# Performance work log

Measured on AMD Instinct MI355X. Metric: run time of the kernel, lower is better.

Reference implementation:

```python
import jax, jax.numpy as jnp
import numpy as np

E, HE, HD, V, B, S, T = 512, 1024, 1024, 32000, 64, 48, 48
PAD = 0


def lstm_cell(x, h, c, Wih, Whh, b):
    # torch gate order: i, f, g, o
    g = x @ Wih.T + h @ Whh.T + b
    i, f, gg, o = jnp.split(g, 4, axis=-1)
    c2 = jax.nn.sigmoid(f) * c + jax.nn.sigmoid(i) * jnp.tanh(gg)
    h2 = jax.nn.sigmoid(o) * jnp.tanh(c2)
    return h2, c2


def run_lstm(X, mask, Wih, Whh, b):
    # X: [S,B,E], mask: [S,B] bool; emulates packed-sequence semantics:
    # carry frozen and output zeroed at padded steps.
    hsz = Whh.shape[1]
    h0 = jnp.zeros((X.shape[1], hsz), X.dtype)

    def step(carry, xm):
        h, c = carry
        x, m = xm
        h2, c2 = lstm_cell(x, h, c, Wih, Whh, b)
        m = m[:, None]
        h = jnp.where(m, h2, h)
        c = jnp.where(m, c2, c)
        return (h, c), h * m

    (hT, cT), outs = jax.lax.scan(step, (h0, h0), (X, mask))
    return outs, hT, cT


def setup_inputs() -> dict:
    key = jax.random.key(0)
    ks = jax.random.split(key, 24)

    def rn(k, shape, scale=0.05):
        return jax.random.normal(k, shape, jnp.float32) * scale

    inp = {}
    inp['source_padded'] = jax.random.randint(ks[0], (S, B), 1, V).astype(jnp.int32)
    inp['target_padded'] = jax.random.randint(ks[1], (T, B), 1, V).astype(jnp.int32)
    lens = jnp.sort(jax.random.randint(ks[2], (B,), S // 2, S + 1))[::-1]
    inp['source_lengths'] = lens.at[0].set(S).astype(jnp.int32)
    # embeddings (padding row zeroed, matching nn.Embedding padding_idx)
    inp['src_emb'] = rn(ks[3], (V, E)).at[PAD].set(0.0)
    inp['tgt_emb'] = rn(ks[4], (V, E)).at[PAD].set(0.0)
    # bidirectional encoder LSTM (b = b_ih + b_hh combined)
    inp['enc_Wih_f'] = rn(ks[5], (4 * HE, E))
    inp['enc_Whh_f'] = rn(ks[6], (4 * HE, HE))
    inp['enc_b_f'] = rn(ks[7], (4 * HE,))
    inp['enc_Wih_b'] = rn(ks[8], (4 * HE, E))
    inp['enc_Whh_b'] = rn(ks[9], (4 * HE, HE))
    inp['enc_b_b'] = rn(ks[10], (4 * HE,))
    # decoder LSTMCell
    inp['dec_Wih'] = rn(ks[11], (4 * HD, E + HD))
    inp['dec_Whh'] = rn(ks[12], (4 * HD, HD))
    inp['dec_b'] = rn(ks[13], (4 * HD,))
    # projections (all bias=False in the original)
    inp['W_h'] = rn(ks[14], (HD, 2 * HE))
    inp['W_c'] = rn(ks[15], (HD, 2 * HE))
    inp['W_att'] = rn(ks[16], (HD, 2 * HE))
    inp['W_comb'] = rn(ks[17], (HE, 2 * HE + HD))
    inp['W_vocab'] = rn(ks[18], (V, HD))
    return inp


def reference(source_padded, target_padded, source_lengths, src_emb, tgt_emb,
              enc_Wih_f, enc_Whh_f, enc_b_f, enc_Wih_b, enc_Whh_b, enc_b_b,
              dec_Wih, dec_Whh, dec_b, W_h, W_c, W_att, W_comb, W_vocab):
    # ---- encode ----
    X = src_emb[source_padded]                       # [S,B,E]
    tpos = jnp.arange(S)[:, None]
    valid = tpos < source_lengths[None, :]           # [S,B]
    fwd_out, h_f, c_f = run_lstm(X, valid, enc_Wih_f, enc_Whh_f, enc_b_f)
    # reverse each sequence within its true length (packed-seq backward dir)
    rev_idx = jnp.where(valid, source_lengths[None, :] - 1 - tpos, tpos)
    Xrev = jnp.take_along_axis(X, rev_idx[:, :, None], axis=0)
    bwd_rev, h_b, c_b = run_lstm(Xrev, valid, enc_Wih_b, enc_Whh_b, enc_b_b)
    bwd_out = jnp.take_along_axis(bwd_rev, rev_idx[:, :, None], axis=0)
    enc_hiddens = jnp.concatenate([fwd_out, bwd_out], -1).transpose(1, 0, 2)  # [B,S,2HE]
    dec_h0 = jnp.concatenate([h_f, h_b], -1) @ W_h.T  # [B,HD]
    dec_c0 = jnp.concatenate([c_f, c_b], -1) @ W_c.T
    # ---- decode ----
    enc_proj = enc_hiddens @ W_att.T                 # [B,S,HD]
    pad_mask = ~valid.T                              # [B,S], True at padding
    Y = tgt_emb[target_padded[:-1]]                  # [T-1,B,E]

    def dstep(o_prev, y):
        ybar = jnp.concatenate([y, o_prev], -1)
        # NOTE: faithful to source bug - step() is always called with
        # dec_init_state, so the LSTMCell state resets every timestep.
        h_t, c_t = lstm_cell(ybar, dec_h0, dec_c0, dec_Wih, dec_Whh, dec_b)
        e = jnp.einsum('bsh,bh->bs', enc_proj, h_t)  # multiplicative attention
        e = jnp.where(pad_mask, -jnp.inf, e)
        alpha = jax.nn.softmax(e, -1)
        a = jnp.einsum('bs,bsd->bd', alpha, enc_hiddens)   # [B,2HE]
        O = jnp.tanh(jnp.concatenate([a, h_t], -1) @ W_comb.T)  # dropout=identity (eval)
        return O, O

    o0 = jnp.zeros((B, HD), X.dtype)
    _, combined = jax.lax.scan(dstep, o0, Y)          # [T-1,B,HE]
    # ---- loss-style scores ----
    P = jax.nn.log_softmax(combined @ W_vocab.T, -1)  # [T-1,B,V]
    gold = jnp.take_along_axis(P, target_padded[1:][:, :, None], axis=-1)[..., 0]
    tmask = (target_padded[1:] != PAD).astype(P.dtype)
    return (gold * tmask).sum(0)                      # [B]
```

## Files before the change

kernel.cpp:

```cpp
#include <hip/hip_runtime.h>
#include <math.h>


#define S_    48
#define B_    64
#define E_    512
#define H_    1024
#define H4_   4096
#define V_    32000
#define T1_   47
#define NROW_ 3008
#define NROWP 3072
#define NTV_  500
#define NBE   128
#define NBD   128

typedef __bf16 bf16x8 __attribute__((ext_vector_type(8)));
typedef float  f32x4  __attribute__((ext_vector_type(4)));
typedef unsigned short ushort_t;
typedef unsigned long long ull_t;

__device__ __forceinline__ float sigm(float x){ return 1.f/(1.f+expf(-x)); }
__device__ __forceinline__ unsigned short f2bs(float f){
  unsigned u=__float_as_uint(f); u+=0x7fffu+((u>>16)&1u); return (unsigned short)(u>>16);
}
__device__ __forceinline__ float b2f(ushort_t u){ return __uint_as_float(((unsigned)u)<<16); }
__device__ __forceinline__ void gload16(const ushort_t* g, ushort_t* l){
  __builtin_amdgcn_global_load_lds((const __attribute__((address_space(1))) void*)g,
                                   (__attribute__((address_space(3))) void*)l,16,0,0);
}

__device__ __forceinline__ void ast32(void* p, unsigned v){
  __hip_atomic_store((unsigned*)p,v,__ATOMIC_RELAXED,__HIP_MEMORY_SCOPE_AGENT);
}
__device__ __forceinline__ void ast64(void* p, ull_t v){
  __hip_atomic_store((ull_t*)p,v,__ATOMIC_RELAXED,__HIP_MEMORY_SCOPE_AGENT);
}

__device__ __forceinline__ void arrive(unsigned* flags, int idx, unsigned ep){
  if(threadIdx.x==0) ast32(&flags[idx*16], ep);
}
__device__ __forceinline__ void wait_flags(unsigned* flags, int n, unsigned ep){
  for(int i=threadIdx.x;i<n;i+=256){
    while(__hip_atomic_load(&flags[i*16],__ATOMIC_RELAXED,__HIP_MEMORY_SCOPE_AGENT)<ep)
      __builtin_amdgcn_s_sleep(1);
  }
  __syncthreads();
}

__device__ __forceinline__ void stage128(const ushort_t* src, int ld, int k0,
                                         ushort_t* lds, int w, int lane){
  const int rA=lane>>3, gA=lane&7;
#pragma unroll
  for(int i=0;i<4;i++){
    int rb=w*32+i*8;
    int row=rb+rA;
    gload16(src+(size_t)row*ld+k0+(((gA)^(row&7))*8), &lds[rb*64]);
  }
}
__device__ __forceinline__ void stage256(const ushort_t* src, int ld, int k0,
                                         ushort_t* lds, int w, int lane){
#pragma unroll
  for(int p=0;p<2;p++){
    int s0=p*1024+w*64;
    int s=s0+lane;
    int row=s>>3, g=s&7;
    gload16(src+(size_t)row*ld+k0+((g^(row&7))*8), &lds[(size_t)s0*8]);
  }
}

#define ACC_DECL \
  f32x4 c00={0,0,0,0},c01={0,0,0,0},c02={0,0,0,0},c03={0,0,0,0}, \
        c10={0,0,0,0},c11={0,0,0,0},c12={0,0,0,0},c13={0,0,0,0}, \
        c20={0,0,0,0},c21={0,0,0,0},c22={0,0,0,0},c23={0,0,0,0}, \
        c30={0,0,0,0},c31={0,0,0,0},c32={0,0,0,0},c33={0,0,0,0};

#define MFMA_ __builtin_amdgcn_mfma_f32_16x16x32_bf16
#define MMA_K64(AsB,BsB) do{ \
  _Pragma("unroll") \
  for(int ks_=0;ks_<2;ks_++){ \
    const int sw_=((ks_*4+l4)^l7)*8; \
    bf16x8 a0_=*(const bf16x8*)&(AsB)[(wm*64+ 0+l15)*64+sw_]; \
    bf16x8 a1_=*(const bf16x8*)&(AsB)[(wm*64+16+l15)*64+sw_]; \
    bf16x8 a2_=*(const bf16x8*)&(AsB)[(wm*64+32+l15)*64+sw_]; \
    bf16x8 a3_=*(const bf16x8*)&(AsB)[(wm*64+48+l15)*64+sw_]; \
    bf16x8 b0_=*(const bf16x8*)&(BsB)[(wn*64+ 0+l15)*64+sw_]; \
    bf16x8 b1_=*(const bf16x8*)&(BsB)[(wn*64+16+l15)*64+sw_]; \
    bf16x8 b2_=*(const bf16x8*)&(BsB)[(wn*64+32+l15)*64+sw_]; \
    bf16x8 b3_=*(const bf16x8*)&(BsB)[(wn*64+48+l15)*64+sw_]; \
    c00=MFMA_(a0_,b0_,c00,0,0,0); c01=MFMA_(a0_,b1_,c01,0,0,0); \
    c02=MFMA_(a0_,b2_,c02,0,0,0); c03=MFMA_(a0_,b3_,c03,0,0,0); \
    c10=MFMA_(a1_,b0_,c10,0,0,0); c11=MFMA_(a1_,b1_,c11,0,0,0); \
    c12=MFMA_(a1_,b2_,c12,0,0,0); c13=MFMA_(a1_,b3_,c13,0,0,0); \
    c20=MFMA_(a2_,b0_,c20,0,0,0); c21=MFMA_(a2_,b1_,c21,0,0,0); \
    c22=MFMA_(a2_,b2_,c22,0,0,0); c23=MFMA_(a2_,b3_,c23,0,0,0); \
    c30=MFMA_(a3_,b0_,c30,0,0,0); c31=MFMA_(a3_,b1_,c31,0,0,0); \
    c32=MFMA_(a3_,b2_,c32,0,0,0); c33=MFMA_(a3_,b3_,c33,0,0,0); \
  } \
}while(0)

__global__ __launch_bounds__(256)
void proj3(const ushort_t* __restrict__ Xb, const ushort_t* __restrict__ WfB, const float* __restrict__ bf,
           const ushort_t* __restrict__ XrB, const ushort_t* __restrict__ WbB, const float* __restrict__ bb,
           const ushort_t* __restrict__ Yb, const ushort_t* __restrict__ WyB,
           ushort_t* __restrict__ XpF, ushort_t* __restrict__ XpB, ushort_t* __restrict__ Yp)
{
  __shared__ __align__(16) ushort_t As[128*64];
  __shared__ __align__(16) ushort_t Bs[128*64];
  const ushort_t* A; const ushort_t* B; const float* bias; ushort_t* C;
  if(blockIdx.z==0){A=Xb;B=WfB;bias=bf;C=XpF;}
  else if(blockIdx.z==1){A=XrB;B=WbB;bias=bb;C=XpB;}
  else {A=Yb;B=WyB;bias=nullptr;C=Yp;}
  const int tid=threadIdx.x, w=tid>>6, lane=tid&63;
  const int wm=w>>1, wn=w&1;
  const int l15=lane&15, l4=lane>>4, l7=lane&7;
  const int m0=blockIdx.x*128, n0=blockIdx.y*128;
  ACC_DECL
  for(int k0=0;k0<E_;k0+=64){
    stage128(A+(size_t)m0*E_, E_, k0, As, w, lane);
    stage128(B+(size_t)n0*E_, E_, k0, Bs, w, lane);
    __syncthreads();
    MMA_K64(As,Bs);
    __syncthreads();
  }
  const int cr=l4*4, cc=l15;
#define PSTORE(CM,mi,ni) { int col=n0+wn*64+(ni)*16+cc; float bv=bias?bias[col]:0.f; \
  _Pragma("unroll") for(int j=0;j<4;j++){ int row=m0+wm*64+(mi)*16+cr+j; \
    C[(size_t)row*H4_+col]=f2bs(CM[j]+bv); } }
  PSTORE(c00,0,0) PSTORE(c01,0,1) PSTORE(c02,0,2) PSTORE(c03,0,3)
  PSTORE(c10,1,0) PSTORE(c11,1,1) PSTORE(c12,1,2) PSTORE(c13,1,3)
  PSTORE(c20,2,0) PSTORE(c21,2,1) PSTORE(c22,2,2) PSTORE(c23,2,3)
  PSTORE(c30,3,0) PSTORE(c31,3,1) PSTORE(c32,3,2) PSTORE(c33,3,3)
#undef PSTORE
}

__global__ __launch_bounds__(256)
void bproj(const ushort_t* __restrict__ A, int lda,
           const ushort_t* __restrict__ B, int ldb, int K,
           ushort_t* __restrict__ Cb)
{
  __shared__ __align__(16) ushort_t As[128*64];
  __shared__ __align__(16) ushort_t Bs[128*64];
  const int tid=threadIdx.x, w=tid>>6, lane=tid&63;
  const int wm=w>>1, wn=w&1;
  const int l15=lane&15, l4=lane>>4, l7=lane&7;
  const int m0=blockIdx.x*128, n0=blockIdx.y*128;
  ACC_DECL
  for(int k0=0;k0<K;k0+=64){
    stage128(A+(size_t)m0*lda, lda, k0, As, w, lane);
    stage128(B+(size_t)n0*ldb, ldb, k0, Bs, w, lane);
    __syncthreads();
    MMA_K64(As,Bs);
    __syncthreads();
  }
  const int cr=l4*4, cc=l15;
#define BSTORE(CM,mi,ni) { int col=n0+wn*64+(ni)*16+cc; \
  _Pragma("unroll") for(int j=0;j<4;j++){ int row=m0+wm*64+(mi)*16+cr+j; \
    Cb[(size_t)row*H_+col]=f2bs(CM[j]); } }
  BSTORE(c00,0,0) BSTORE(c01,0,1) BSTORE(c02,0,2) BSTORE(c03,0,3)
  BSTORE(c10,1,0) BSTORE(c11,1,1) BSTORE(c12,1,2) BSTORE(c13,1,3)
  BSTORE(c20,2,0) BSTORE(c21,2,1) BSTORE(c22,2,2) BSTORE(c23,2,3)
  BSTORE(c30,3,0) BSTORE(c31,3,1) BSTORE(c32,3,2) BSTORE(c33,3,3)
#undef BSTORE
}

__global__ __launch_bounds__(1024)
void mfma_vocab(const ushort_t* __restrict__ A, const ushort_t* __restrict__ B,
                const int* __restrict__ tgt,
                float* __restrict__ pmax, float* __restrict__ psum, float* __restrict__ gold)
{
  __shared__ __align__(16) ushort_t As[256*64];
  __shared__ __align__(16) ushort_t Bs[256*64];
  const int tid=threadIdx.x, w=tid>>6, lane=tid&63;
  const int wm=w>>2, wn=w&3;
  const int l15=lane&15, l4=lane>>4, l7=lane&7;
  const int m0=blockIdx.x*256, n0=blockIdx.y*256;
  ACC_DECL
  for(int k0=0;k0<H_;k0+=64){
    stage256(A+(size_t)m0*H_, H_, k0, As, w, lane);
    stage256(B+(size_t)n0*H_, H_, k0, Bs, w, lane);
    __syncthreads();
    MMA_K64(As,Bs);
    __syncthreads();
  }
  const int tile=blockIdx.y*4+wn;
  const int cc=l15;
#define VEPI(mi,R0,R1,R2,R3) { \
  _Pragma("unroll") for(int j=0;j<4;j++){ \
    int row=m0+wm*64+(mi)*16+l4*4+j; \
    float m=fmaxf(fmaxf(R0[j],R1[j]),fmaxf(R2[j],R3[j])); \
    for(int o=1;o<16;o<<=1) m=fmaxf(m,__shfl_xor(m,o,64)); \
    float s=expf(R0[j]-m)+expf(R1[j]-m)+expf(R2[j]-m)+expf(R3[j]-m); \
    for(int o=1;o<16;o<<=1) s+=__shfl_xor(s,o,64); \
    if(row<NROW_){ \
      if(cc==0){ pmax[(size_t)tile*NROWP+row]=m; psum[(size_t)tile*NROWP+row]=s; } \
      int g=tgt[((row>>6)+1)*B_+(row&63)]; \
      int lj=g-(n0+wn*64); \
      if(lj>=0&&lj<64&&(lj&15)==cc){ int q=lj>>4; \
        gold[row]= (q==0)?R0[j]:(q==1)?R1[j]:(q==2)?R2[j]:R3[j]; } \
    } } }
  VEPI(0,c00,c01,c02,c03)
  VEPI(1,c10,c11,c12,c13)
  VEPI(2,c20,c21,c22,c23)
  VEPI(3,c30,c31,c32,c33)
#undef VEPI
}

__global__ __launch_bounds__(256)
void enc_persist(const ushort_t* __restrict__ WhhB2,
                 const ushort_t* __restrict__ XpF, const ushort_t* __restrict__ XpB,
                 const int* __restrict__ lens,
                 ushort_t* __restrict__ hroll,
                 float* __restrict__ cst,
                 ushort_t* __restrict__ outF, ushort_t* __restrict__ outBR,
                 unsigned* __restrict__ flagsE)
{
  __shared__ __align__(16) ushort_t Bp[64*1024];
  const int tid=threadIdx.x, w=tid>>6, lane=tid&63;
  const int blk=blockIdx.x, dir=blk>>6, j0=(blk&63)*16;
  const int l15=lane&15, l4=lane>>4;
  const ushort_t* Wd=WhhB2+(size_t)dir*H4_*H_;
  const ushort_t* xp = dir? XpB : XpF;
  float* cD = cst + (size_t)dir*65536;
  ushort_t* outD = dir? outBR : outF;
  unsigned* fD = flagsE + dir*64*16;

  for(int p=0;p<32;p++){
    int s=p*256+w*64+lane;
    int row=s>>7, g=s&127;
    int grow=((row>>4)<<10)+j0+(row&15);
    gload16(Wd+(size_t)grow*H_+((g^(row&7))*8), &Bp[(p*256+w*64)*8]);
  }
  __syncthreads();

  float hkeep[4]={0.f,0.f,0.f,0.f};

  for(int t=0;t<S_;t++){
    const ushort_t* hbR = hroll + ((size_t)t*2+dir)*65536;
    ushort_t*       hbW = hroll + ((size_t)(t+1)*2+dir)*65536;
    bf16x8 a[32];
    {
      const ushort_t* ap=hbR+(size_t)(w*16+l15)*H_+l4*8;
#pragma unroll
      for(int kk=0;kk<32;kk++) a[kk]=*(const bf16x8*)(ap+kk*32);
    }
    f32x4 acc[4];
#pragma unroll
    for(int n=0;n<4;n++) acc[n]=(f32x4){0.f,0.f,0.f,0.f};
#pragma unroll
    for(int kk=0;kk<32;kk++){
#pragma unroll
      for(int n=0;n<4;n++){
        int rb=n*16+l15;
        bf16x8 b=*(const bf16x8*)&Bp[rb*H_+(((kk*4+l4)^(rb&7))*8)];
        acc[n]=__builtin_amdgcn_mfma_f32_16x16x32_bf16(a[kk],b,acc[n],0,0,0);
      }
    }
    const int col=j0+l15;
#pragma unroll
    for(int j=0;j<4;j++){
      int row=w*16+l4*4+j;
      const ushort_t* xr=xp+(size_t)(t*64+row)*H4_;
      float g0=acc[0][j]+b2f(xr[col]);
      float g1=acc[1][j]+b2f(xr[1024+col]);
      float g2=acc[2][j]+b2f(xr[2048+col]);
      float g3=acc[3][j]+b2f(xr[3072+col]);
      size_t ix=(size_t)row*H_+col;
      float c_old=cD[ix];
      float cn=sigm(g1)*c_old+sigm(g0)*tanhf(g2);
      float hv=sigm(g3)*tanhf(cn);
      bool m=t<lens[row];
      cD[ix]= m? cn : c_old;
      hkeep[j]= m? hv : hkeep[j];
      outD[(size_t)(t*64+row)*H_+col]= m? f2bs(hv) : (ushort_t)0;
      ushort_t h16=f2bs(hkeep[j]);
      ushort_t other=(ushort_t)__shfl_xor((int)h16,1,64);
      if((lane&1)==0)
        ast32((void*)(hbW+ix), (unsigned)h16 | ((unsigned)other<<16));
    }
    __syncthreads();
    arrive(fD, blk&63, (unsigned)(t+1));
    wait_flags(fD, 64, (unsigned)(t+1));
  }
}

__global__ __launch_bounds__(256)
void dec_persist(const ushort_t* __restrict__ WoB,
                 const ushort_t* __restrict__ Yp,
                 const float* __restrict__ whhC,
                 const float* __restrict__ dc0,
                 const ushort_t* __restrict__ encPb,
                 const ushort_t* __restrict__ Gb,
                 const ushort_t* __restrict__ WcombB,
                 const int* __restrict__ lens,
                 ushort_t* __restrict__ opRoll,
                 ushort_t* __restrict__ hRoll,
                 float* __restrict__ accRoll,
                 ushort_t* __restrict__ combB,
                 unsigned* __restrict__ fA,
                 unsigned* __restrict__ fB,
                 unsigned* __restrict__ fM)
{
  __shared__ __align__(16) ushort_t Bp[32*1024];
  __shared__ __align__(16) ushort_t WcHp[16*1024];
  __shared__ float gbuf[64*32];
  __shared__ float whhCs[64*32];
  __shared__ float dc0s[64*8];
  __shared__ float es[S_], al[S_];
  const int tid=threadIdx.x, w=tid>>6, lane=tid&63;
  const int blk=blockIdx.x;
  const int l15=lane&15, l4=lane>>4;
  const int j0=blk*8;
  const int b=blk;
  const int j0c=(blk-64)*16;

  for(int p=0;p<16;p++){
    int s=p*256+w*64+lane;
    int row=s>>7, g=s&127;
    int grow=((row>>3)<<10)+j0+(row&7);
    gload16(WoB+(size_t)grow*H_+((g^(row&7))*8), &Bp[(p*256+w*64)*8]);
  }
  if(blk>=64){
    for(int p=0;p<8;p++){
      int s=p*256+w*64+lane;
      int row=s>>7, g=s&127;
      gload16(WcombB+(size_t)(j0c+row)*3072+2048+((g^(row&7))*8), &WcHp[(p*256+w*64)*8]);
    }
  }
  for(int p=0;p<8;p++){
    int s=p*256+tid;
    int row=s>>5, gc=s&31, gate=gc>>3, c=gc&7;
    whhCs[s]=whhC[(size_t)row*H4_+gate*1024+j0+c];
  }
  if(tid<512){ int row=tid>>3, c=tid&7; dc0s[tid]=dc0[(size_t)row*H_+j0+c]; }
  __syncthreads();

  for(int t=0;t<T1_;t++){
    const unsigned ept=(unsigned)(t+1);
    const ushort_t* opT = opRoll + (size_t)t*65536;
    ushort_t*       opW = opRoll + (size_t)(t+1)*65536;
    ushort_t*       hT  = hRoll  + (size_t)t*65536;
    float*          accT= accRoll+ (size_t)t*65536;
    {
      bf16x8 a[32];
      {
        const ushort_t* ap=opT+(size_t)(w*16+l15)*H_+l4*8;
#pragma unroll
        for(int kk=0;kk<32;kk++) a[kk]=*(const bf16x8*)(ap+kk*32);
      }
      f32x4 acc0=(f32x4){0.f,0.f,0.f,0.f}, acc1=(f32x4){0.f,0.f,0.f,0.f};
#pragma unroll
      for(int kk=0;kk<32;kk++){
        int rb0=l15, rb1=16+l15;
        bf16x8 b0=*(const bf16x8*)&Bp[rb0*1024+(((kk*4+l4)^(rb0&7))*8)];
        bf16x8 b1=*(const bf16x8*)&Bp[rb1*1024+(((kk*4+l4)^(rb1&7))*8)];
        acc0=__builtin_amdgcn_mfma_f32_16x16x32_bf16(a[kk],b0,acc0,0,0,0);
        acc1=__builtin_amdgcn_mfma_f32_16x16x32_bf16(a[kk],b1,acc1,0,0,0);
      }
#pragma unroll
      for(int j=0;j<4;j++){
        gbuf[(w*16+l4*4+j)*32 + l15   ]=acc0[j];
        gbuf[(w*16+l4*4+j)*32 + 16+l15]=acc1[j];
      }
      __syncthreads();
      {
        int o=tid*2, row=o>>3, c=o&7;
        const ushort_t* ypr=Yp+(size_t)(t*64+row)*H4_;
        float hv2[2];
#pragma unroll
        for(int q=0;q<2;q++){
          int cc=c+q;
          float g0=gbuf[row*32+cc]   +b2f(ypr[j0+cc])     +whhCs[row*32+cc];
          float g1=gbuf[row*32+8+cc] +b2f(ypr[1024+j0+cc])+whhCs[row*32+8+cc];
          float g2=gbuf[row*32+16+cc]+b2f(ypr[2048+j0+cc])+whhCs[row*32+16+cc];
          float g3=gbuf[row*32+24+cc]+b2f(ypr[3072+j0+cc])+whhCs[row*32+24+cc];
          float cn=sigm(g1)*dc0s[row*8+cc]+sigm(g0)*tanhf(g2);
          hv2[q]=sigm(g3)*tanhf(cn);
        }
        unsigned pk=(unsigned)f2bs(hv2[0]) | ((unsigned)f2bs(hv2[1])<<16);
        ast32((void*)(hT+(size_t)row*H_+j0+c), pk);
      }
    }
    __syncthreads();
    arrive(fA, blk, ept);
    wait_flags(fA, 128, ept);

    if(blk<64){
      float hreg[16];
      {
        const ushort_t* hp=hT+(size_t)b*H_+lane*16;
        bf16x8 h0=*(const bf16x8*)hp, h1=*(const bf16x8*)(hp+8);
#pragma unroll
        for(int i=0;i<8;i++){ hreg[i]=b2f(((const ushort_t*)&h0)[i]);
                              hreg[8+i]=b2f(((const ushort_t*)&h1)[i]); }
      }
      for(int s=w;s<S_;s+=4){
        const ushort_t* epr=encPb+((size_t)b*S_+s)*H_+lane*16;
        bf16x8 e0=*(const bf16x8*)epr, e1=*(const bf16x8*)(epr+8);
        float sum=0.f;
#pragma unroll
        for(int i=0;i<8;i++) sum+=b2f(((const ushort_t*)&e0)[i])*hreg[i]
                                +b2f(((const ushort_t*)&e1)[i])*hreg[8+i];
        for(int o=32;o>0;o>>=1) sum+=__shfl_xor(sum,o,64);
        if(lane==0) es[s]=sum;
      }
      __syncthreads();
      if(tid<64){
        int L=lens[b];
        float e=(tid<S_&&tid<L)? es[tid] : -INFINITY;
        float m=e;
        for(int o=32;o>0;o>>=1) m=fmaxf(m,__shfl_xor(m,o,64));
        float p=(tid<S_)? expf(e-m):0.f;
        float sm=p;
        for(int o=32;o>0;o>>=1) sm+=__shfl_xor(sm,o,64);
        if(tid<S_) al[tid]=p/sm;
      }
      __syncthreads();
      float r0=0.f,r1=0.f,r2=0.f,r3=0.f;
      const int c4=tid*4;
      for(int s=0;s<S_;s++){
        float aa=al[s];
        ushort4 g4=*(const ushort4*)(Gb+((size_t)b*S_+s)*H_+c4);
        r0+=aa*b2f(g4.x); r1+=aa*b2f(g4.y); r2+=aa*b2f(g4.z); r3+=aa*b2f(g4.w);
      }
      wait_flags(fM, 64, ept);
      {
        float4 ap4=*(const float4*)(accT+(size_t)b*H_+c4);
        float o0=tanhf(r0+ap4.x);
        float o1=tanhf(r1+ap4.y);
        float o2=tanhf(r2+ap4.z);
        float o3=tanhf(r3+ap4.w);
        ushort_t b0=f2bs(o0),b1=f2bs(o1),b2_=f2bs(o2),b3=f2bs(o3);
        ull_t pk=(ull_t)b0 | ((ull_t)b1<<16) | ((ull_t)b2_<<32) | ((ull_t)b3<<48);
        ast64((void*)(opW+(size_t)b*H_+c4), pk);
        ushort4 cb; cb.x=b0; cb.y=b1; cb.z=b2_; cb.w=b3;
        *(ushort4*)(combB+((size_t)t*64+b)*H_+c4)=cb;
      }
      __syncthreads();
      arrive(fB, blk, ept);
      wait_flags(fB, 64, ept);
    } else {
      bf16x8 a[32];
      {
        const ushort_t* ap=hT+(size_t)(w*16+l15)*H_+l4*8;
#pragma unroll
        for(int kk=0;kk<32;kk++) a[kk]=*(const bf16x8*)(ap+kk*32);
      }
      f32x4 accP=(f32x4){0.f,0.f,0.f,0.f};
#pragma unroll
      for(int kk=0;kk<32;kk++){
        bf16x8 bb=*(const bf16x8*)&WcHp[l15*1024+(((kk*4+l4)^(l15&7))*8)];
        accP=__builtin_amdgcn_mfma_f32_16x16x32_bf16(a[kk],bb,accP,0,0,0);
      }
#pragma unroll
      for(int j=0;j<4;j++){
        int row=w*16+l4*4+j, col=j0c+l15;
        float v=accP[j];
        float other=__shfl_xor(v,1,64);
        if((lane&1)==0){
          union{ float f[2]; ull_t q; } u; u.f[0]=v; u.f[1]=other;
          ast64((void*)(accT+(size_t)row*H_+col), u.q);
        }
      }
      __syncthreads();
      arrive(fM, blk-64, ept);
      wait_flags(fB, 64, ept);
    }
  }
}

__global__ void embed_all(const int* __restrict__ src, const int* __restrict__ tgt,
                          const int* __restrict__ lens,
                          const float* __restrict__ se, const float* __restrict__ te,
                          ushort_t* __restrict__ X, ushort_t* __restrict__ Xr,
                          ushort_t* __restrict__ Y)
{
  int bi=blockIdx.x, tid=threadIdx.x;
  const float* srcrow; ushort_t* dst;
  if(bi<3072){
    int s=bi>>6, b=bi&63;
    srcrow=se+(size_t)src[s*64+b]*E_; dst=X+(size_t)bi*E_;
  } else if(bi<6144){
    int r=bi-3072, t=r>>6, b=r&63;
    int L=lens[b]; int ts=(t<L)? L-1-t : t;
    srcrow=se+(size_t)src[ts*64+b]*E_; dst=Xr+(size_t)r*E_;
  } else {
    int r=bi-6144, t=r>>6, b=r&63;
    srcrow=te+(size_t)tgt[t*64+b]*E_; dst=Y+(size_t)r*E_;
  }
  float4 v=((const float4*)srcrow)[tid];
  ushort4 o; o.x=f2bs(v.x); o.y=f2bs(v.y); o.z=f2bs(v.z); o.w=f2bs(v.w);
  ((ushort4*)dst)[tid]=o;
}

__global__ void prep_w(const float* __restrict__ Whhf,const float* __restrict__ Whhb,
                       const float* __restrict__ Wihf,const float* __restrict__ Wihb,
                       const float* __restrict__ Watt,const float* __restrict__ dWih,
                       const float* __restrict__ Wcomb,
                       ushort_t* __restrict__ WhhfB,ushort_t* __restrict__ WhhbB,
                       ushort_t* __restrict__ WihfB,ushort_t* __restrict__ WihbB,
                       ushort_t* __restrict__ WattB,ushort_t* __restrict__ dWihYb,
                       ushort_t* __restrict__ dWihOb,ushort_t* __restrict__ WcombB)
{
  const int NQ=6029312;
  for(int q=blockIdx.x*256+threadIdx.x; q<NQ; q+=gridDim.x*256){
    const float* src; ushort_t* dst; size_t si,di; int r;
    if(q<1048576){ si=(size_t)q*4; src=Whhf; dst=WhhfB; di=si; }
    else if(q<2097152){ r=q-1048576; si=(size_t)r*4; src=Whhb; dst=WhhbB; di=si; }
    else if(q<2621440){ r=q-2097152; si=(size_t)r*4; src=Wihf; dst=WihfB; di=si; }
    else if(q<3145728){ r=q-2621440; si=(size_t)r*4; src=Wihb; dst=WihbB; di=si; }
    else if(q<3670016){ r=q-3145728; si=(size_t)r*4; src=Watt; dst=WattB; di=si; }
    else if(q<4194304){ r=q-3670016; int row=r>>7, c4=(r&127)*4;
                        si=(size_t)row*1536+c4; src=dWih; dst=dWihYb; di=(size_t)row*512+c4; }
    else if(q<5242880){ r=q-4194304; int row=r>>8, c4=(r&255)*4;
                        si=(size_t)row*1536+512+c4; src=dWih; dst=dWihOb; di=(size_t)row*1024+c4; }
    else { r=q-5242880; si=(size_t)r*4; src=Wcomb; dst=WcombB; di=si; }
    float4 v=*(const float4*)(src+si);
    ushort4 o; o.x=f2bs(v.x);o.y=f2bs(v.y);o.z=f2bs(v.z);o.w=f2bs(v.w);
    *(ushort4*)(dst+di)=o;
  }
}

__global__ void f2b_voc(const float* __restrict__ in, ushort_t* __restrict__ out){
  for(size_t q=blockIdx.x*256+threadIdx.x; q<8192000; q+=(size_t)gridDim.x*256){
    float4 v=*(const float4*)(in+q*4);
    ushort4 o; o.x=f2bs(v.x);o.y=f2bs(v.y);o.z=f2bs(v.z);o.w=f2bs(v.w);
    *(ushort4*)(out+q*4)=o;
  }
}

__global__ void gather_concat(const ushort_t* __restrict__ outF, const ushort_t* __restrict__ outBR,
                              const int* __restrict__ lens,
                              const ushort_t* __restrict__ hb, const float* __restrict__ cst,
                              ushort_t* __restrict__ encHb,
                              float* __restrict__ hcat, float* __restrict__ ccat)
{
  int bi=blockIdx.x, tid=threadIdx.x;
  if(bi<3072){
    int b=bi/48, s=bi%48;
    int L=lens[b]; int sr=(s<L)? L-1-s : s;
    ((ushort4*)(encHb+(size_t)bi*2048))[tid]      =((const ushort4*)(outF +(size_t)(s*64+b)*H_))[tid];
    ((ushort4*)(encHb+(size_t)bi*2048+1024))[tid] =((const ushort4*)(outBR+(size_t)(sr*64+b)*H_))[tid];
  } else {
    int b=bi-3072;
    for(int i=tid;i<H_;i+=256){
      hcat[(size_t)b*2048+i]      = b2f(hb[(size_t)b*H_+i]);
      hcat[(size_t)b*2048+1024+i] = b2f(hb[65536+(size_t)b*H_+i]);
      ccat[(size_t)b*2048+i]      = cst[(size_t)b*H_+i];
      ccat[(size_t)b*2048+1024+i] = cst[65536+(size_t)b*H_+i];
    }
  }
}

template<int BM,int BN,int TM,int TN>
__global__ __launch_bounds__(256)
void gemm_nt(int M, int K,
             const float* __restrict__ A, int lda,
             const float* __restrict__ B, int ldb,
             float* __restrict__ C, int ldc,
             const float* __restrict__ bias)
{
  constexpr int BK=16;
  __shared__ float As[BK][BM+4];
  __shared__ float Bs[BK][BN+4];
  const int tid=threadIdx.x;
  constexpr int TX=BN/TN;
  const int tx=tid%TX, ty=tid/TX;
  const int m0=blockIdx.x*BM, n0=blockIdx.y*BN;
  float acc[TM][TN];
#pragma unroll
  for(int i=0;i<TM;i++)
#pragma unroll
    for(int j=0;j<TN;j++) acc[i][j]=0.f;
  for(int k0=0;k0<K;k0+=BK){
    for(int i=tid;i<BM*4;i+=256){
      int r=i>>2, c=(i&3)*4;
      float4 v=make_float4(0.f,0.f,0.f,0.f);
      if(m0+r<M) v=*(const float4*)(A+(size_t)(m0+r)*lda+k0+c);
      As[c+0][r]=v.x; As[c+1][r]=v.y; As[c+2][r]=v.z; As[c+3][r]=v.w;
    }
    for(int i=tid;i<BN*4;i+=256){
      int r=i>>2, c=(i&3)*4;
      float4 v=*(const float4*)(B+(size_t)(n0+r)*ldb+k0+c);
      Bs[c+0][r]=v.x; Bs[c+1][r]=v.y; Bs[c+2][r]=v.z; Bs[c+3][r]=v.w;
    }
    __syncthreads();
#pragma unroll
    for(int k=0;k<BK;k++){
      float a[TM], bb[TN];
#pragma unroll
      for(int i=0;i<TM;i++) a[i]=As[k][ty*TM+i];
#pragma unroll
      for(int j=0;j<TN;j++) bb[j]=Bs[k][tx*TN+j];
#pragma unroll
      for(int i=0;i<TM;i++)
#pragma unroll
        for(int j=0;j<TN;j++) acc[i][j]+=a[i]*bb[j];
    }
    __syncthreads();
  }
#pragma unroll
  for(int i=0;i<TM;i++){
    int r=m0+ty*TM+i;
    if(r>=M) continue;
#pragma unroll
    for(int j=0;j<TN;j++){
      int c=n0+tx*TN+j;
      float v=acc[i][j];
      if(bias) v+=bias[c];
      C[(size_t)r*ldc+c]=v;
    }
  }
}

__global__ __launch_bounds__(256)
void lse_final(const float* __restrict__ pmax, const float* __restrict__ psum,
               const float* __restrict__ gold, float* __restrict__ gl)
{
  int r=blockIdx.x*256+threadIdx.x;
  if(r>=NROW_) return;
  float M=-INFINITY, S=0.f;
  for(int i=0;i<NTV_;i++){
    float m2=pmax[(size_t)i*NROWP+r];
    float s2=psum[(size_t)i*NROWP+r];
    float Mn=fmaxf(M,m2);
    S = S*expf(M-Mn) + s2*expf(m2-Mn);
    M=Mn;
  }
  gl[r]=gold[r]-(M+logf(S));
}

__global__ void final_sum(const float* __restrict__ gl, const int* __restrict__ tgt,
                          float* __restrict__ out)
{
  int b=threadIdx.x;
  float acc=0.f;
  for(int t=0;t<T1_;t++){
    int tk=tgt[(t+1)*B_+b];
    if(tk!=0) acc+=gl[t*B_+b];
  }
  out[b]=acc;
}

extern "C" void kernel_launch(void* const* d_in, const int* in_sizes, int n_in,
                              void* d_out, int out_size, void* d_ws, size_t ws_size,
                              hipStream_t stream)
{
  (void)in_sizes; (void)n_in; (void)out_size; (void)ws_size;
  const int*   src    =(const int*)  d_in[0];
  const int*   tgt    =(const int*)  d_in[1];
  const int*   lens   =(const int*)  d_in[2];
  const float* src_emb=(const float*)d_in[3];
  const float* tgt_emb=(const float*)d_in[4];
  const float* Wih_f  =(const float*)d_in[5];
  const float* Whh_f  =(const float*)d_in[6];
  const float* b_f    =(const float*)d_in[7];
  const float* Wih_b  =(const float*)d_in[8];
  const float* Whh_b  =(const float*)d_in[9];
  const float* b_b    =(const float*)d_in[10];
  const float* dWih   =(const float*)d_in[11];
  const float* dWhh   =(const float*)d_in[12];
  const float* db     =(const float*)d_in[13];
  const float* W_h    =(const float*)d_in[14];
  const float* W_c    =(const float*)d_in[15];
  const float* W_att  =(const float*)d_in[16];
  const float* W_comb =(const float*)d_in[17];
  const float* W_voc  =(const float*)d_in[18];
  float* out=(float*)d_out;
  float* W  =(float*)d_ws;

  size_t off=0;
  auto AL=[&](size_t n){ size_t o=off; off+=n; return o; };
  const size_t oXpF  =AL((size_t)3072*H4_);
  const size_t oXpB  =AL((size_t)3072*H4_);
  const size_t oYp   =AL((size_t)3072*H4_);
  const size_t oCst  =AL((size_t)2*64*H_);
  const size_t oHcat =AL((size_t)64*2048);
  const size_t oCcat =AL((size_t)64*2048);
  const size_t oDh0  =AL((size_t)64*H_);
  const size_t oDc0  =AL((size_t)64*H_);
  const size_t oWhhC =AL((size_t)64*H4_);
  const size_t oBar  =AL((size_t)8192);
  const size_t oXb    =AL((size_t)3072*E_/2);
  const size_t oXrb   =AL((size_t)3072*E_/2);
  const size_t oYb    =AL((size_t)3072*E_/2);
  const size_t oWhhfB =AL((size_t)H4_*H_/2);
  const size_t oWhhbB =AL((size_t)H4_*H_/2);
  const size_t oWihfB =AL((size_t)H4_*E_/2);
  const size_t oWihbB =AL((size_t)H4_*E_/2);
  const size_t oWattB =AL((size_t)H_*2048/2);
  const size_t odWihYb=AL((size_t)H4_*E_/2);
  const size_t odWihOb=AL((size_t)H4_*H_/2);
  const size_t oWcombB=AL((size_t)H_*3072/2);
  const size_t oOutF  =AL((size_t)S_*64*H_/2);
  const size_t oOutBR =AL((size_t)S_*64*H_/2);
  const size_t oEncHb =AL((size_t)3072*2048/2);
  const size_t oEncPb =AL((size_t)3072*H_/2);

  ushort_t* Xb    =(ushort_t*)(W+oXb);
  ushort_t* Xrb   =(ushort_t*)(W+oXrb);
  ushort_t* Yb    =(ushort_t*)(W+oYb);
  ushort_t* WhhfB =(ushort_t*)(W+oWhhfB);
  ushort_t* WihfB =(ushort_t*)(W+oWihfB);
  ushort_t* WihbB =(ushort_t*)(W+oWihbB);
  ushort_t* WattB =(ushort_t*)(W+oWattB);
  ushort_t* dWihYb=(ushort_t*)(W+odWihYb);
  ushort_t* dWihOb=(ushort_t*)(W+odWihOb);
  ushort_t* WcombB=(ushort_t*)(W+oWcombB);
  ushort_t* OutF  =(ushort_t*)(W+oOutF);
  ushort_t* OutBR =(ushort_t*)(W+oOutBR);
  ushort_t* EncHb =(ushort_t*)(W+oEncHb);
  ushort_t* EncPb =(ushort_t*)(W+oEncPb);
  ushort_t* XpFb  =(ushort_t*)(W+oXpF);
  ushort_t* XpBb  =(ushort_t*)(W+oXpB);
  ushort_t* YpB   =(ushort_t*)(W+oYp);
  float*    AccRoll = W+oYp+6300000;
  ushort_t* WvocB =(ushort_t*)(W+oXpF);
  float* pmax = W+oXpF+16450000;
  float* psum = pmax + (size_t)NTV_*NROWP;
  ushort_t* Gbuf  =(ushort_t*)(W+oXpF+19550000);
  ushort_t* OpRoll=(ushort_t*)(W+oXpF+21150000);
  ushort_t* HRoll =(ushort_t*)(W+oXpF+22750000);
  float* gold = W+oXpF+24400000;
  float* gl   = gold + NROWP;
  ushort_t* HrollE=EncHb;
  ushort_t* HbFin =HrollE+(size_t)S_*2*65536;
  ushort_t* CombB =(ushort_t*)(W+oOutF);
  unsigned* flagsE=(unsigned*)(W+oBar);
  unsigned* fA = flagsE + 2*64*16;
  unsigned* fB = fA + 128*16;
  unsigned* fM = fB + 64*16;

  hipMemsetAsync(W+oBar, 0, 8192*sizeof(float), stream);
  hipMemsetAsync(W+oCst, 0, (size_t)2*64*H_*sizeof(float), stream);
  hipMemsetAsync(HrollE, 0, (size_t)2*65536*sizeof(ushort_t), stream);

  embed_all<<<dim3(3072+3072+NROW_),128,0,stream>>>(src,tgt,lens,src_emb,tgt_emb,Xb,Xrb,Yb);
  prep_w<<<dim3(2048),256,0,stream>>>(Whh_f,Whh_b,Wih_f,Wih_b,W_att,dWih,W_comb,
                                      WhhfB,(ushort_t*)(W+oWhhbB),WihfB,WihbB,WattB,
                                      dWihYb,dWihOb,WcombB);
  proj3<<<dim3(24,32,3),256,0,stream>>>(Xb,WihfB,b_f, Xrb,WihbB,b_b, Yb,dWihYb,
                                        XpFb,XpBb,YpB);

  enc_persist<<<dim3(NBE),256,0,stream>>>(WhhfB, XpFb, XpBb, lens,
                                          HrollE, W+oCst, OutF, OutBR, flagsE);

  hipMemsetAsync(OpRoll, 0, (size_t)65536*sizeof(ushort_t), stream);

  gather_concat<<<dim3(3136),256,0,stream>>>(OutF,OutBR,lens,HbFin,W+oCst,
                                             EncHb,W+oHcat,W+oCcat);
  f2b_voc<<<dim3(2048),256,0,stream>>>(W_voc, WvocB);
  bproj<<<dim3(24,8),256,0,stream>>>(EncHb,2048, WattB,2048, 2048, EncPb);
  bproj<<<dim3(24,8),256,0,stream>>>(EncHb,2048, WcombB,3072, 2048, Gbuf);
  gemm_nt<64,64,4,4><<<dim3(1,16),256,0,stream>>>(64,2048, W+oHcat,2048, W_h,2048, W+oDh0,H_, nullptr);
  gemm_nt<64,64,4,4><<<dim3(1,16),256,0,stream>>>(64,2048, W+oCcat,2048, W_c,2048, W+oDc0,H_, nullptr);
  gemm_nt<64,64,4,4><<<dim3(1,64),256,0,stream>>>(64,H_, W+oDh0,H_, dWhh,H_, W+oWhhC,H4_, db);

  dec_persist<<<dim3(NBD),256,0,stream>>>(dWihOb, YpB, W+oWhhC, W+oDc0,
                                          EncPb, Gbuf, WcombB, lens,
                                          OpRoll, HRoll, AccRoll, CombB, fA, fB, fM);

  mfma_vocab<<<dim3(12,125),1024,0,stream>>>(CombB, WvocB, tgt, pmax, psum, gold);
  lse_final<<<dim3((NROW_+255)/256),256,0,stream>>>(pmax, psum, gold, gl);
  final_sum<<<dim3(1),64,0,stream>>>(gl, tgt, out);
}
```

Baseline: 2.214 ms.

## Fuse vocab projection into persistent decoder kernel to overlap with recurrence

Removes the separate mfma_vocab launch and adds 125 extra blocks to dec_persist. Each of these blocks owns a 256-column stripe of the vocab weight and, once a decoder step's flag is published, computes that step's 64-row logits tile with its partial max, sum and gold values. The aim is to hide the large vocab GEMM behind the sequential decoder recurrence instead of running it afterwards. The combined-output store becomes an atomic 64-bit store so the consumer blocks see it. The risks are that the vocab blocks re-stream the whole vocab weight every step (47 times in total) rather than reusing it across rows, they compete with the latency-critical decoder blocks for bandwidth, and the persistent grid now depends on all 253 blocks being co-resident.

```diff
diff --git a/kernel.cpp b/kernel.cpp
--- a/kernel.cpp
+++ b/kernel.cpp
@@ -14,6 +14,7 @@
 #define NTV_  500
 #define NBE   128
 #define NBD   128
+#define NVB   125
 
 typedef __bf16 bf16x8 __attribute__((ext_vector_type(8)));
 typedef float  f32x4  __attribute__((ext_vector_type(4)));
@@ -56,16 +57,6 @@
     int rb=w*32+i*8;
     int row=rb+rA;
     gload16(src+(size_t)row*ld+k0+(((gA)^(row&7))*8), &lds[rb*64]);
-  }
-}
-__device__ __forceinline__ void stage256(const ushort_t* src, int ld, int k0,
-                                         ushort_t* lds, int w, int lane){
-#pragma unroll
-  for(int p=0;p<2;p++){
-    int s0=p*1024+w*64;
-    int s=s0+lane;
-    int row=s>>3, g=s&7;
-    gload16(src+(size_t)row*ld+k0+((g^(row&7))*8), &lds[(size_t)s0*8]);
   }
 }
 
@@ -164,48 +155,6 @@
 #undef BSTORE
 }
 
-__global__ __launch_bounds__(1024)
-void mfma_vocab(const ushort_t* __restrict__ A, const ushort_t* __restrict__ B,
-                const int* __restrict__ tgt,
-                float* __restrict__ pmax, float* __restrict__ psum, float* __restrict__ gold)
-{
-  __shared__ __align__(16) ushort_t As[256*64];
-  __shared__ __align__(16) ushort_t Bs[256*64];
-  const int tid=threadIdx.x, w=tid>>6, lane=tid&63;
-  const int wm=w>>2, wn=w&3;
-  const int l15=lane&15, l4=lane>>4, l7=lane&7;
-  const int m0=blockIdx.x*256, n0=blockIdx.y*256;
-  ACC_DECL
-  for(int k0=0;k0<H_;k0+=64){
-    stage256(A+(size_t)m0*H_, H_, k0, As, w, lane);
-    stage256(B+(size_t)n0*H_, H_, k0, Bs, w, lane);
-    __syncthreads();
-    MMA_K64(As,Bs);
-    __syncthreads();
-  }
-  const int tile=blockIdx.y*4+wn;
-  const int cc=l15;
-#define VEPI(mi,R0,R1,R2,R3) { \
-  _Pragma("unroll") for(int j=0;j<4;j++){ \
-    int row=m0+wm*64+(mi)*16+l4*4+j; \
-    float m=fmaxf(fmaxf(R0[j],R1[j]),fmaxf(R2[j],R3[j])); \
-    for(int o=1;o<16;o<<=1) m=fmaxf(m,__shfl_xor(m,o,64)); \
-    float s=expf(R0[j]-m)+expf(R1[j]-m)+expf(R2[j]-m)+expf(R3[j]-m); \
-    for(int o=1;o<16;o<<=1) s+=__shfl_xor(s,o,64); \
-    if(row<NROW_){ \
-      if(cc==0){ pmax[(size_t)tile*NROWP+row]=m; psum[(size_t)tile*NROWP+row]=s; } \
-      int g=tgt[((row>>6)+1)*B_+(row&63)]; \
-      int lj=g-(n0+wn*64); \
-      if(lj>=0&&lj<64&&(lj&15)==cc){ int q=lj>>4; \
-        gold[row]= (q==0)?R0[j]:(q==1)?R1[j]:(q==2)?R2[j]:R3[j]; } \
-    } } }
-  VEPI(0,c00,c01,c02,c03)
-  VEPI(1,c10,c11,c12,c13)
-  VEPI(2,c20,c21,c22,c23)
-  VEPI(3,c30,c31,c32,c33)
-#undef VEPI
-}
-
 __global__ __launch_bounds__(256)
 void enc_persist(const ushort_t* __restrict__ WhhB2,
                  const ushort_t* __restrict__ XpF, const ushort_t* __restrict__ XpB,
@@ -297,6 +246,10 @@
                  ushort_t* __restrict__ hRoll,
                  float* __restrict__ accRoll,
                  ushort_t* __restrict__ combB,
+                 const ushort_t* __restrict__ WvocB,
+                 const int* __restrict__ tgt,
+                 float* __restrict__ pmax, float* __restrict__ psum,
+                 float* __restrict__ gold,
                  unsigned* __restrict__ fA,
                  unsigned* __restrict__ fB,
                  unsigned* __restrict__ fM)
@@ -309,7 +262,59 @@
   __shared__ float es[S_], al[S_];
   const int tid=threadIdx.x, w=tid>>6, lane=tid&63;
   const int blk=blockIdx.x;
-  const int l15=lane&15, l4=lane>>4;
+  const int l15=lane&15, l4=lane>>4, l7=lane&7;
+
+  if(blk>=NBD){
+    const int stripe=blk-NBD;
+    ushort_t* As=(ushort_t*)Bp;
+    ushort_t* Bs=((ushort_t*)Bp)+64*64;
+    const int n0=stripe*256;
+    const ushort_t* Bv=WvocB+(size_t)n0*H_;
+    const int wm=0, wn=w;
+    const int cc=l15;
+    for(int t=0;t<T1_;t++){
+      wait_flags(fB, 64, (unsigned)(t+1));
+      const ushort_t* Ap=combB+(size_t)t*64*H_;
+      ACC_DECL
+      for(int k0=0;k0<H_;k0+=64){
+#pragma unroll
+        for(int p=0;p<2;p++){
+          int s0=p*256+w*64; int s=s0+lane; int row=s>>3, g=s&7;
+          gload16(Ap+(size_t)row*H_+k0+((g^(row&7))*8), &As[(size_t)s0*8]);
+        }
+#pragma unroll
+        for(int p=0;p<8;p++){
+          int s0=p*256+w*64; int s=s0+lane; int row=s>>3, g=s&7;
+          gload16(Bv+(size_t)row*H_+k0+((g^(row&7))*8), &Bs[(size_t)s0*8]);
+        }
+        __syncthreads();
+        MMA_K64(As,Bs);
+        __syncthreads();
+      }
+      const int tile=stripe*4+w;
+#define VVEPI(mi,R0,R1,R2,R3) { \
+      _Pragma("unroll") for(int j=0;j<4;j++){ \
+        int row=t*64+(mi)*16+l4*4+j; \
+        float m=fmaxf(fmaxf(R0[j],R1[j]),fmaxf(R2[j],R3[j])); \
+        for(int o=1;o<16;o<<=1) m=fmaxf(m,__shfl_xor(m,o,64)); \
+        float s=expf(R0[j]-m)+expf(R1[j]-m)+expf(R2[j]-m)+expf(R3[j]-m); \
+        for(int o=1;o<16;o<<=1) s+=__shfl_xor(s,o,64); \
+        if(cc==0){ pmax[(size_t)tile*NROWP+row]=m; psum[(size_t)tile*NROWP+row]=s; } \
+        int g=tgt[(t+1)*B_+(row&63)]; \
+        int lj=g-(n0+w*64); \
+        if(lj>=0&&lj<64&&(lj&15)==cc){ int q=lj>>4; \
+          gold[row]= (q==0)?R0[j]:(q==1)?R1[j]:(q==2)?R2[j]:R3[j]; } \
+      } }
+      VVEPI(0,c00,c01,c02,c03)
+      VVEPI(1,c10,c11,c12,c13)
+      VVEPI(2,c20,c21,c22,c23)
+      VVEPI(3,c30,c31,c32,c33)
+#undef VVEPI
+      __syncthreads();
+    }
+    return;
+  }
+
   const int j0=blk*8;
   const int b=blk;
   const int j0c=(blk-64)*16;
@@ -433,8 +438,7 @@
         ushort_t b0=f2bs(o0),b1=f2bs(o1),b2_=f2bs(o2),b3=f2bs(o3);
         ull_t pk=(ull_t)b0 | ((ull_t)b1<<16) | ((ull_t)b2_<<32) | ((ull_t)b3<<48);
         ast64((void*)(opW+(size_t)b*H_+c4), pk);
-        ushort4 cb; cb.x=b0; cb.y=b1; cb.z=b2_; cb.w=b3;
-        *(ushort4*)(combB+((size_t)t*64+b)*H_+c4)=cb;
+        ast64((void*)(combB+((size_t)t*64+b)*H_+c4), pk);
       }
       __syncthreads();
       arrive(fB, blk, ept);
@@ -756,11 +760,12 @@
   gemm_nt<64,64,4,4><<<dim3(1,16),256,0,stream>>>(64,2048, W+oCcat,2048, W_c,2048, W+oDc0,H_, nullptr);
   gemm_nt<64,64,4,4><<<dim3(1,64),256,0,stream>>>(64,H_, W+oDh0,H_, dWhh,H_, W+oWhhC,H4_, db);
 
-  dec_persist<<<dim3(NBD),256,0,stream>>>(dWihOb, YpB, W+oWhhC, W+oDc0,
-                                          EncPb, Gbuf, WcombB, lens,
-                                          OpRoll, HRoll, AccRoll, CombB, fA, fB, fM);
-
-  mfma_vocab<<<dim3(12,125),1024,0,stream>>>(CombB, WvocB, tgt, pmax, psum, gold);
+  dec_persist<<<dim3(NBD+NVB),256,0,stream>>>(dWihOb, YpB, W+oWhhC, W+oDc0,
+                                              EncPb, Gbuf, WcombB, lens,
+                                              OpRoll, HRoll, AccRoll, CombB,
+                                              WvocB, tgt, pmax, psum, gold,
+                                              fA, fB, fM);
+
   lse_final<<<dim3((NROW_+255)/256),256,0,stream>>>(pmax, psum, gold, gl);
   final_sum<<<dim3(1),64,0,stream>>>(gl, tgt, out);
 }
```

After: 2.570 ms. 16.1% more time.
